# Kernel optimization log

Hardware: AMD Instinct MI355X
Metric: run time of the kernel (lower is better)

## Reference

```python
import jax, jax.numpy as jnp
import numpy as np

C = 1.0                      # curvature
PHI = 3.1415926 * 0.3        # Cosine phase (bias=False path)
ALPHA = 0.2                  # LeakyReLU negative slope
A_PARA = 0.5                 # a_para_GATLayer
EPS = 4e-3                   # float32 ball-projection epsilon (standard HGCN)
MIN_NORM = 1e-15
NEG_INF = -9e15              # matches -9000000000000000.0 in source


def project(x, c):
    # clamp points to lie inside the Poincare ball of curvature c
    norm = jnp.maximum(jnp.linalg.norm(x, axis=-1, keepdims=True), MIN_NORM)
    maxnorm = (1.0 - EPS) / jnp.sqrt(c)
    return jnp.where(norm > maxnorm, x / norm * maxnorm, x)


def artanh(x):
    return jnp.arctanh(jnp.clip(x, -1.0 + 1e-7, 1.0 - 1e-7))


def logmap0(p, c):
    # log map at the origin of the Poincare ball
    sqrt_c = c ** 0.5
    p_norm = jnp.maximum(jnp.linalg.norm(p, axis=-1, keepdims=True), MIN_NORM)
    return artanh(sqrt_c * p_norm) / (sqrt_c * p_norm) * p


def setup_inputs() -> dict:
    key = jax.random.key(0)
    k1, k2, k3, k4 = jax.random.split(key, 4)
    N, FIN, FOUT = 8192, 512, 128
    h = jax.random.normal(k1, (N, FIN), dtype=jnp.float32)
    adj = jax.random.randint(k2, (N, N), 0, 2, dtype=jnp.int32)
    # xavier_uniform with gain=1.414
    lim_w = 1.414 * np.sqrt(6.0 / (FIN + FOUT))
    W = jax.random.uniform(k3, (FIN, FOUT), jnp.float32, -lim_w, lim_w)
    lim_a = 1.414 * np.sqrt(6.0 / (2 * FOUT + 1))
    a = jax.random.uniform(k4, (2 * FOUT, 1), jnp.float32, -lim_a, lim_a)
    return {"h": h, "adj": adj, "W": W, "a": a}


def reference(h, adj, W, a):
    fout = W.shape[1]
    Wh = h @ W                                   # [N, F_out]
    Wh1 = Wh @ a[:fout]                          # [N, 1] source score
    Wh2 = Wh @ a[fout:]                          # [N, 1] target score
    e = jax.nn.leaky_relu(Wh1 + Wh2.T, ALPHA)    # [N, N]
    e = jnp.where(adj > 0, e, NEG_INF)
    attention = jax.nn.softmax(e, axis=1)        # dropout p=0 (eval): identity
    h_prime = attention @ Wh                     # [N, F_out]
    h_prime = logmap0(project(h_prime, C), C)
    # concat=True branch: ELU + a_para * A*cos(x + phi), A=1 (data_dim=-1)
    return jax.nn.elu(h_prime) + A_PARA * jnp.cos(h_prime + PHI)
```

## Files before the change

### kernel.cpp

```cpp
#include <hip/hip_runtime.h>
#include <hip/hip_bf16.h>
#include <math.h>

typedef short short8 __attribute__((ext_vector_type(8)));
typedef float f32x4 __attribute__((ext_vector_type(4)));

static constexpr int N = 8192;
static constexpr int FIN = 512;
static constexpr int FOUT = 128;
static constexpr float PHI = 3.1415926f * 0.3f;
static constexpr float A_PARA = 0.5f;
static constexpr float EPS_BALL = 4e-3f;
static constexpr float L2E = 1.4426950408889634f;

__device__ __forceinline__ unsigned short f2b(float f) {
    union { float f; unsigned u; } v; v.f = f;
    unsigned r = v.u + 0x7fffu + ((v.u >> 16) & 1u);
    return (unsigned short)(r >> 16);
}

__device__ __forceinline__ unsigned f2key(float x) {
    unsigned b = __float_as_uint(x);
    return (b & 0x80000000u) ? ~b : (b | 0x80000000u);
}
__device__ __forceinline__ float key2f(unsigned k) {
    unsigned b = (k & 0x80000000u) ? (k ^ 0x80000000u) : ~k;
    return __uint_as_float(b);
}

__device__ __forceinline__ short8 cvt8(float4 x0, float4 x1) {
    short8 r;
    r[0] = (short)f2b(x0.x); r[1] = (short)f2b(x0.y);
    r[2] = (short)f2b(x0.z); r[3] = (short)f2b(x0.w);
    r[4] = (short)f2b(x1.x); r[5] = (short)f2b(x1.y);
    r[6] = (short)f2b(x1.z); r[7] = (short)f2b(x1.w);
    return r;
}

__device__ __forceinline__ void cw(float* w, const int4 a, const float4 tv,
                                   float sA, float mA) {
    float z;
    z = sA + tv.x; w[0] = a.x > 0 ? __builtin_amdgcn_exp2f(fmaxf(z, 0.2f * z) - mA) : 0.f;
    z = sA + tv.y; w[1] = a.y > 0 ? __builtin_amdgcn_exp2f(fmaxf(z, 0.2f * z) - mA) : 0.f;
    z = sA + tv.z; w[2] = a.z > 0 ? __builtin_amdgcn_exp2f(fmaxf(z, 0.2f * z) - mA) : 0.f;
    z = sA + tv.w; w[3] = a.w > 0 ? __builtin_amdgcn_exp2f(fmaxf(z, 0.2f * z) - mA) : 0.f;
}

__global__ __launch_bounds__(256) void k0_wt(const float* __restrict__ W,
                                             unsigned short* __restrict__ Wt) {
    __shared__ float sh[32][33];
    const int t = threadIdx.x;
    const int k0 = (blockIdx.x >> 2) * 32, c0 = (blockIdx.x & 3) * 32;
    {
        int r = t >> 3, c4 = (t & 7) * 4;
        float4 v = *(const float4*)(W + (size_t)(k0 + r) * FOUT + c0 + c4);
        sh[r][c4] = v.x; sh[r][c4 + 1] = v.y; sh[r][c4 + 2] = v.z; sh[r][c4 + 3] = v.w;
    }
    __syncthreads();
    int cc = t >> 3, k4 = (t & 7) * 4;
    ushort4 o;
    o.x = f2b(sh[k4][cc]); o.y = f2b(sh[k4 + 1][cc]);
    o.z = f2b(sh[k4 + 2][cc]); o.w = f2b(sh[k4 + 3][cc]);
    *(ushort4*)(Wt + (size_t)(c0 + cc) * FIN + k0 + k4) = o;
}

__global__ __launch_bounds__(256) void k1_gemm(
    const float* __restrict__ h, const unsigned short* __restrict__ Wt,
    const float* __restrict__ a, unsigned short* __restrict__ whbt,
    float* __restrict__ s_out, float* __restrict__ t_out,
    unsigned* __restrict__ Tkey)
{
    __shared__ unsigned short hsb[2][32][72];
    __shared__ float sred[32][2], tred[32][2];
    const int t = threadIdx.x, lane = t & 63, wave = t >> 6;
    const int i0 = blockIdx.x * 32;
    const int wr = wave & 1, wc = wave >> 1;
    const int arow = lane & 15, g = lane >> 4;
    const int sr = t >> 3, sc = (t & 7) * 8;
    const float* hp = h + (size_t)(i0 + sr) * FIN + sc;

    float4 x0 = *(const float4*)hp, x1 = *(const float4*)(hp + 4);
    *(short8*)&hsb[0][sr][sc] = cvt8(x0, x1);
    __syncthreads();

    f32x4 acc[4];
    const f32x4 zz = {0.f, 0.f, 0.f, 0.f};
    #pragma unroll
    for (int cf = 0; cf < 4; ++cf) acc[cf] = zz;

    #pragma unroll 1
    for (int kt = 0; kt < 8; ++kt) {
        const int cur = kt & 1;
        float4 y0, y1;
        if (kt < 7) {
            y0 = *(const float4*)(hp + (kt + 1) * 64);
            y1 = *(const float4*)(hp + (kt + 1) * 64 + 4);
        }
        #pragma unroll
        for (int js = 0; js < 64; js += 32) {
            short8 af = *(const short8*)&hsb[cur][wr * 16 + arow][js + g * 8];
            #pragma unroll
            for (int cf = 0; cf < 4; ++cf) {
                const unsigned short* bp =
                    Wt + (size_t)(wc * 64 + cf * 16 + arow) * FIN + kt * 64 + js + g * 8;
                short8 bf = *(const short8*)bp;
                acc[cf] = __builtin_amdgcn_mfma_f32_16x16x32_bf16(af, bf, acc[cf], 0, 0, 0);
            }
        }
        if (kt < 7) {
            *(short8*)&hsb[cur ^ 1][sr][sc] = cvt8(y0, y1);
            __syncthreads();
        }
    }

    float a1v[4], a2v[4];
    #pragma unroll
    for (int cf = 0; cf < 4; ++cf) {
        int col = wc * 64 + cf * 16 + arow;
        a1v[cf] = a[col]; a2v[cf] = a[FOUT + col];
    }
    #pragma unroll
    for (int cf = 0; cf < 4; ++cf) {
        int col = wc * 64 + cf * 16 + arow;
        ushort4 o;
        o.x = f2b(acc[cf][0]); o.y = f2b(acc[cf][1]);
        o.z = f2b(acc[cf][2]); o.w = f2b(acc[cf][3]);
        *(ushort4*)(whbt + (size_t)col * N + i0 + wr * 16 + g * 4) = o;
    }
    #pragma unroll
    for (int q = 0; q < 4; ++q) {
        float sp = acc[0][q]*a1v[0] + acc[1][q]*a1v[1] + acc[2][q]*a1v[2] + acc[3][q]*a1v[3];
        float tp = acc[0][q]*a2v[0] + acc[1][q]*a2v[1] + acc[2][q]*a2v[2] + acc[3][q]*a2v[3];
        #pragma unroll
        for (int m = 1; m < 16; m <<= 1) {
            sp += __shfl_xor(sp, m, 16);
            tp += __shfl_xor(tp, m, 16);
        }
        if (arow == 0) {
            sred[wr * 16 + g * 4 + q][wc] = sp;
            tred[wr * 16 + g * 4 + q][wc] = tp;
        }
    }
    __syncthreads();
    if (t < 32) {
        float sp = (sred[t][0] + sred[t][1]) * L2E;
        float tp = (tred[t][0] + tred[t][1]) * L2E;
        s_out[i0 + t] = sp;
        t_out[i0 + t] = tp;
        float m = tp;
        #pragma unroll
        for (int d = 1; d < 32; d <<= 1) m = fmaxf(m, __shfl_xor(m, d, 32));
        if (t == 0) atomicMax(Tkey, f2key(m));
    }
}

__global__ __launch_bounds__(512, 4) void k3_attn(
    const int* __restrict__ adj, const unsigned short* __restrict__ whbt,
    const float* __restrict__ s_in, const float* __restrict__ t_in,
    const unsigned* __restrict__ Tkey,
    unsigned short* __restrict__ num_bf, float* __restrict__ num_f32,
    float* __restrict__ den_out, int slice_mode)
{
    __shared__ unsigned short bt[2][128][72];
    __shared__ float tl[1024];
    const int t = threadIdx.x, lane = t & 63, wave = t >> 6;
    const int jc = blockIdx.x & 7, it = blockIdx.x >> 3;
    const int i0 = it * 128, jbase = jc * 1024;

    tl[t] = t_in[jbase + t];
    tl[t + 512] = t_in[jbase + t + 512];

    const int arow = lane & 15, g = lane >> 4;
    const int grow = i0 + wave * 16 + arow;
    const float sA = s_in[grow];
    const float Tv = key2f(Tkey[0]);
    const float zT = sA + Tv;
    const float mA = fmaxf(zT, 0.2f * zT);
    const int* adjrow = adj + (size_t)grow * N;
    const int srow = t >> 2, scol = (t & 3) * 16;
    const unsigned short* sbase = whbt + (size_t)srow * N + jbase + scol;

    f32x4 acc[8];
    const f32x4 zz = {0.f, 0.f, 0.f, 0.f};
    #pragma unroll
    for (int c = 0; c < 8; ++c) acc[c] = zz;
    float den = 0.f;

    short8 sr0 = *(const short8*)sbase;
    short8 sr1 = *(const short8*)(sbase + 8);
    int4 av0 = *(const int4*)(adjrow + jbase + g * 8);
    int4 av1 = *(const int4*)(adjrow + jbase + g * 8 + 4);
    int4 av2 = *(const int4*)(adjrow + jbase + 32 + g * 8);
    int4 av3 = *(const int4*)(adjrow + jbase + 32 + g * 8 + 4);
    *(short8*)&bt[0][srow][scol]     = sr0;
    *(short8*)&bt[0][srow][scol + 8] = sr1;
    __syncthreads();

    #pragma unroll 1
    for (int jt = 0; jt < 16; ++jt) {
        const int cur = jt & 1, jl = jt * 64;
        float4 ta = *(const float4*)&tl[jl + g * 8];
        float4 tb = *(const float4*)&tl[jl + g * 8 + 4];
        float4 tc = *(const float4*)&tl[jl + 32 + g * 8];
        float4 td = *(const float4*)&tl[jl + 32 + g * 8 + 4];
        int4 an0, an1, an2, an3; short8 n0, n1;
        if (jt < 15) {
            const int* ap = adjrow + jbase + jl + 64;
            an0 = *(const int4*)(ap + g * 8);
            an1 = *(const int4*)(ap + g * 8 + 4);
            an2 = *(const int4*)(ap + 32 + g * 8);
            an3 = *(const int4*)(ap + 32 + g * 8 + 4);
            const unsigned short* p = sbase + (jt + 1) * 64;
            n0 = *(const short8*)p;
            n1 = *(const short8*)(p + 8);
        }
        float w[16];
        cw(&w[0],  av0, ta, sA, mA);
        cw(&w[4],  av1, tb, sA, mA);
        cw(&w[8],  av2, tc, sA, mA);
        cw(&w[12], av3, td, sA, mA);
        #pragma unroll
        for (int e = 0; e < 16; ++e) den += w[e];
        short8 af0, af1;
        #pragma unroll
        for (int e = 0; e < 8; ++e) {
            af0[e] = (short)f2b(w[e]);
            af1[e] = (short)f2b(w[8 + e]);
        }
        #pragma unroll
        for (int c = 0; c < 8; ++c) {
            short8 bf = *(const short8*)&bt[cur][c * 16 + arow][g * 8];
            acc[c] = __builtin_amdgcn_mfma_f32_16x16x32_bf16(af0, bf, acc[c], 0, 0, 0);
        }
        #pragma unroll
        for (int c = 0; c < 8; ++c) {
            short8 bf = *(const short8*)&bt[cur][c * 16 + arow][32 + g * 8];
            acc[c] = __builtin_amdgcn_mfma_f32_16x16x32_bf16(af1, bf, acc[c], 0, 0, 0);
        }
        if (jt < 15) {
            *(short8*)&bt[cur ^ 1][srow][scol]     = n0;
            *(short8*)&bt[cur ^ 1][srow][scol + 8] = n1;
            av0 = an0; av1 = an1; av2 = an2; av3 = an3;
            __syncthreads();
        }
    }

    den += __shfl_xor(den, 16, 64);
    den += __shfl_xor(den, 32, 64);
    if (g == 0) atomicAdd(&den_out[grow], den);

    const int orow0 = i0 + wave * 16;
    if (slice_mode) {
        unsigned short* dst = num_bf + (size_t)jc * ((size_t)N * FOUT);
        #pragma unroll
        for (int c = 0; c < 8; ++c)
            #pragma unroll
            for (int q = 0; q < 4; ++q)
                dst[(size_t)(orow0 + g * 4 + q) * FOUT + c * 16 + arow] = f2b(acc[c][q]);
    } else {
        #pragma unroll
        for (int c = 0; c < 8; ++c)
            #pragma unroll
            for (int q = 0; q < 4; ++q)
                atomicAdd(&num_f32[(size_t)(orow0 + g * 4 + q) * FOUT + c * 16 + arow], acc[c][q]);
    }
}

__global__ __launch_bounds__(256) void k4_epi(
    const unsigned short* __restrict__ numb, const float* __restrict__ numf,
    const float* __restrict__ den, float* __restrict__ out, int bfmode)
{
    const int row = blockIdx.x * 16 + (threadIdx.x >> 4);
    const int l = threadIdx.x & 15;
    const float inv = 1.0f / den[row];
    float v[8]; float ss = 0.f;
    #pragma unroll
    for (int c = 0; c < 8; ++c) {
        float x = 0.f;
        if (bfmode) {
            for (int s5 = 0; s5 < 8; ++s5) {
                unsigned b = numb[(size_t)s5 * N * FOUT + (size_t)row * FOUT + c * 16 + l];
                x += __uint_as_float(b << 16);
            }
        } else {
            x = numf[(size_t)row * FOUT + c * 16 + l];
        }
        v[c] = x * inv;
        ss += v[c] * v[c];
    }
    #pragma unroll
    for (int m = 1; m < 16; m <<= 1) ss += __shfl_xor(ss, m, 16);
    float nrm = sqrtf(ss);
    const float maxn = 1.0f - EPS_BALL;
    float scale1 = nrm > maxn ? maxn / nrm : 1.0f;
    float pn = fminf(nrm, maxn);
    float fac;
    if (pn < 1e-6f) fac = scale1;
    else fac = scale1 * (0.5f * __logf((1.f + pn) / (1.f - pn))) / pn;
    #pragma unroll
    for (int c = 0; c < 8; ++c) {
        float hv = v[c] * fac;
        float eluv = hv > 0.f ? hv : __expf(hv) - 1.f;
        out[(size_t)row * FOUT + c * 16 + l] = eluv + A_PARA * __cosf(hv + PHI);
    }
}

extern "C" void kernel_launch(void* const* d_in, const int* in_sizes, int n_in,
                              void* d_out, int out_size, void* d_ws, size_t ws_size,
                              hipStream_t stream) {
    const float* h   = (const float*)d_in[0];
    const int*   adj = (const int*)d_in[1];
    const float* W   = (const float*)d_in[2];
    const float* a   = (const float*)d_in[3];
    float* out = (float*)d_out;

    char* ws = (char*)d_ws;
    unsigned short* whbt = (unsigned short*)ws;
    size_t off = (size_t)N * FOUT * 2;
    unsigned short* Wt = (unsigned short*)(ws + off); off += (size_t)FOUT * FIN * 2;
    float* s  = (float*)(ws + off); off += (size_t)N * 4;
    float* tt = (float*)(ws + off); off += (size_t)N * 4;
    unsigned* Tkey = (unsigned*)(ws + off); off += 256;
    float* denb = (float*)(ws + off); off += (size_t)N * 4;
    const size_t slice_bytes = (size_t)N * FOUT * 2;
    const bool fast = ws_size >= off + 8 * slice_bytes;
    unsigned short* numb = fast ? (unsigned short*)(ws + off) : nullptr;

    hipMemsetAsync(Tkey, 0, 4, stream);
    hipMemsetAsync(denb, 0, (size_t)N * 4, stream);
    if (!fast) hipMemsetAsync(out, 0, (size_t)N * FOUT * 4, stream);

    k0_wt<<<64, 256, 0, stream>>>(W, Wt);
    k1_gemm<<<N / 32, 256, 0, stream>>>(h, Wt, a, whbt, s, tt, Tkey);
    k3_attn<<<512, 512, 0, stream>>>(adj, whbt, s, tt, Tkey, numb, out, denb, fast ? 1 : 0);
    k4_epi<<<N / 16, 256, 0, stream>>>(numb, out, denb, out, fast ? 1 : 0);
}
```

Baseline: 104.4 us.

## Fold memsets into W transpose, retile GEMM, deepen adj prefetch, vectorize epilogue

Zeroing of Tkey and the denominator buffer moves into the W-transpose kernel, which removes two memset launches. The projection GEMM now uses 16-row blocks with the whole K-slice of h staged in LDS and no inner barriers, giving twice as many blocks. The attention kernel prefetches adjacency two tiles ahead instead of one, at the cost of more registers. The epilogue reads bf16 slices and writes its output as 8-wide vectors instead of strided scalars.

```diff
diff --git a/kernel.cpp b/kernel.cpp
--- a/kernel.cpp
+++ b/kernel.cpp
@@ -47,7 +47,9 @@
 }
 
 __global__ __launch_bounds__(256) void k0_wt(const float* __restrict__ W,
-                                             unsigned short* __restrict__ Wt) {
+                                             unsigned short* __restrict__ Wt,
+                                             unsigned* __restrict__ Tkey,
+                                             float* __restrict__ denb) {
     __shared__ float sh[32][33];
     const int t = threadIdx.x;
     const int k0 = (blockIdx.x >> 2) * 32, c0 = (blockIdx.x & 3) * 32;
@@ -62,94 +64,84 @@
     o.x = f2b(sh[k4][cc]); o.y = f2b(sh[k4 + 1][cc]);
     o.z = f2b(sh[k4 + 2][cc]); o.w = f2b(sh[k4 + 3][cc]);
     *(ushort4*)(Wt + (size_t)(c0 + cc) * FIN + k0 + k4) = o;
-}
-
-__global__ __launch_bounds__(256) void k1_gemm(
+    if (blockIdx.x == 0) {
+        if (t == 0) Tkey[0] = 0u;
+        for (int i = t; i < N; i += 256) denb[i] = 0.f;
+    }
+}
+
+__global__ __launch_bounds__(256, 2) void k1_gemm(
     const float* __restrict__ h, const unsigned short* __restrict__ Wt,
     const float* __restrict__ a, unsigned short* __restrict__ whbt,
     float* __restrict__ s_out, float* __restrict__ t_out,
     unsigned* __restrict__ Tkey)
 {
-    __shared__ unsigned short hsb[2][32][72];
-    __shared__ float sred[32][2], tred[32][2];
-    const int t = threadIdx.x, lane = t & 63, wave = t >> 6;
-    const int i0 = blockIdx.x * 32;
-    const int wr = wave & 1, wc = wave >> 1;
+    __shared__ unsigned short hsb[16][520];
+    __shared__ float sred[16][4], tred[16][4];
+    const int t = threadIdx.x, lane = t & 63, wc = t >> 6;
+    const int i0 = blockIdx.x * 16;
     const int arow = lane & 15, g = lane >> 4;
-    const int sr = t >> 3, sc = (t & 7) * 8;
-    const float* hp = h + (size_t)(i0 + sr) * FIN + sc;
-
-    float4 x0 = *(const float4*)hp, x1 = *(const float4*)(hp + 4);
-    *(short8*)&hsb[0][sr][sc] = cvt8(x0, x1);
+
+    {
+        const int r = t >> 4, col0 = (t & 15) * 32;
+        const float* hp = h + (size_t)(i0 + r) * FIN + col0;
+        #pragma unroll
+        for (int u = 0; u < 4; ++u) {
+            float4 x0 = *(const float4*)(hp + u * 8);
+            float4 x1 = *(const float4*)(hp + u * 8 + 4);
+            *(short8*)&hsb[r][col0 + u * 8] = cvt8(x0, x1);
+        }
+    }
     __syncthreads();
 
-    f32x4 acc[4];
+    f32x4 acc[2];
     const f32x4 zz = {0.f, 0.f, 0.f, 0.f};
-    #pragma unroll
-    for (int cf = 0; cf < 4; ++cf) acc[cf] = zz;
-
-    #pragma unroll 1
-    for (int kt = 0; kt < 8; ++kt) {
-        const int cur = kt & 1;
-        float4 y0, y1;
-        if (kt < 7) {
-            y0 = *(const float4*)(hp + (kt + 1) * 64);
-            y1 = *(const float4*)(hp + (kt + 1) * 64 + 4);
-        }
-        #pragma unroll
-        for (int js = 0; js < 64; js += 32) {
-            short8 af = *(const short8*)&hsb[cur][wr * 16 + arow][js + g * 8];
-            #pragma unroll
-            for (int cf = 0; cf < 4; ++cf) {
-                const unsigned short* bp =
-                    Wt + (size_t)(wc * 64 + cf * 16 + arow) * FIN + kt * 64 + js + g * 8;
-                short8 bf = *(const short8*)bp;
-                acc[cf] = __builtin_amdgcn_mfma_f32_16x16x32_bf16(af, bf, acc[cf], 0, 0, 0);
-            }
-        }
-        if (kt < 7) {
-            *(short8*)&hsb[cur ^ 1][sr][sc] = cvt8(y0, y1);
-            __syncthreads();
-        }
-    }
-
-    float a1v[4], a2v[4];
-    #pragma unroll
-    for (int cf = 0; cf < 4; ++cf) {
-        int col = wc * 64 + cf * 16 + arow;
-        a1v[cf] = a[col]; a2v[cf] = a[FOUT + col];
-    }
-    #pragma unroll
-    for (int cf = 0; cf < 4; ++cf) {
-        int col = wc * 64 + cf * 16 + arow;
+    acc[0] = zz; acc[1] = zz;
+    const int col_0 = wc * 32 + arow;
+    const int col_1 = wc * 32 + 16 + arow;
+    const unsigned short* bp0 = Wt + (size_t)col_0 * FIN + g * 8;
+    const unsigned short* bp1 = Wt + (size_t)col_1 * FIN + g * 8;
+
+    #pragma unroll
+    for (int ks = 0; ks < 16; ++ks) {
+        short8 af = *(const short8*)&hsb[arow][ks * 32 + g * 8];
+        short8 b0 = *(const short8*)(bp0 + ks * 32);
+        short8 b1 = *(const short8*)(bp1 + ks * 32);
+        acc[0] = __builtin_amdgcn_mfma_f32_16x16x32_bf16(af, b0, acc[0], 0, 0, 0);
+        acc[1] = __builtin_amdgcn_mfma_f32_16x16x32_bf16(af, b1, acc[1], 0, 0, 0);
+    }
+
+    const float a10 = a[col_0], a11 = a[col_1];
+    const float a20 = a[FOUT + col_0], a21 = a[FOUT + col_1];
+    {
         ushort4 o;
-        o.x = f2b(acc[cf][0]); o.y = f2b(acc[cf][1]);
-        o.z = f2b(acc[cf][2]); o.w = f2b(acc[cf][3]);
-        *(ushort4*)(whbt + (size_t)col * N + i0 + wr * 16 + g * 4) = o;
+        o.x = f2b(acc[0][0]); o.y = f2b(acc[0][1]);
+        o.z = f2b(acc[0][2]); o.w = f2b(acc[0][3]);
+        *(ushort4*)(whbt + (size_t)col_0 * N + i0 + g * 4) = o;
+        o.x = f2b(acc[1][0]); o.y = f2b(acc[1][1]);
+        o.z = f2b(acc[1][2]); o.w = f2b(acc[1][3]);
+        *(ushort4*)(whbt + (size_t)col_1 * N + i0 + g * 4) = o;
     }
     #pragma unroll
     for (int q = 0; q < 4; ++q) {
-        float sp = acc[0][q]*a1v[0] + acc[1][q]*a1v[1] + acc[2][q]*a1v[2] + acc[3][q]*a1v[3];
-        float tp = acc[0][q]*a2v[0] + acc[1][q]*a2v[1] + acc[2][q]*a2v[2] + acc[3][q]*a2v[3];
+        float sp = acc[0][q] * a10 + acc[1][q] * a11;
+        float tp = acc[0][q] * a20 + acc[1][q] * a21;
         #pragma unroll
         for (int m = 1; m < 16; m <<= 1) {
             sp += __shfl_xor(sp, m, 16);
             tp += __shfl_xor(tp, m, 16);
         }
-        if (arow == 0) {
-            sred[wr * 16 + g * 4 + q][wc] = sp;
-            tred[wr * 16 + g * 4 + q][wc] = tp;
-        }
+        if (arow == 0) { sred[g * 4 + q][wc] = sp; tred[g * 4 + q][wc] = tp; }
     }
     __syncthreads();
-    if (t < 32) {
-        float sp = (sred[t][0] + sred[t][1]) * L2E;
-        float tp = (tred[t][0] + tred[t][1]) * L2E;
+    if (t < 16) {
+        float sp = (sred[t][0] + sred[t][1] + sred[t][2] + sred[t][3]) * L2E;
+        float tp = (tred[t][0] + tred[t][1] + tred[t][2] + tred[t][3]) * L2E;
         s_out[i0 + t] = sp;
         t_out[i0 + t] = tp;
         float m = tp;
         #pragma unroll
-        for (int d = 1; d < 32; d <<= 1) m = fmaxf(m, __shfl_xor(m, d, 32));
+        for (int d = 1; d < 16; d <<= 1) m = fmaxf(m, __shfl_xor(m, d, 16));
         if (t == 0) atomicMax(Tkey, f2key(m));
     }
 }
@@ -192,6 +184,10 @@
     int4 av1 = *(const int4*)(adjrow + jbase + g * 8 + 4);
     int4 av2 = *(const int4*)(adjrow + jbase + 32 + g * 8);
     int4 av3 = *(const int4*)(adjrow + jbase + 32 + g * 8 + 4);
+    int4 bv0 = *(const int4*)(adjrow + jbase + 64 + g * 8);
+    int4 bv1 = *(const int4*)(adjrow + jbase + 64 + g * 8 + 4);
+    int4 bv2 = *(const int4*)(adjrow + jbase + 96 + g * 8);
+    int4 bv3 = *(const int4*)(adjrow + jbase + 96 + g * 8 + 4);
     *(short8*)&bt[0][srow][scol]     = sr0;
     *(short8*)&bt[0][srow][scol + 8] = sr1;
     __syncthreads();
@@ -199,21 +195,24 @@
     #pragma unroll 1
     for (int jt = 0; jt < 16; ++jt) {
         const int cur = jt & 1, jl = jt * 64;
+        short8 n0, n1;
+        if (jt < 15) {
+            const unsigned short* p = sbase + (jt + 1) * 64;
+            n0 = *(const short8*)p;
+            n1 = *(const short8*)(p + 8);
+        }
+        int4 zv0, zv1, zv2, zv3;
+        if (jt < 14) {
+            const int* ap = adjrow + jbase + jl + 128;
+            zv0 = *(const int4*)(ap + g * 8);
+            zv1 = *(const int4*)(ap + g * 8 + 4);
+            zv2 = *(const int4*)(ap + 32 + g * 8);
+            zv3 = *(const int4*)(ap + 32 + g * 8 + 4);
+        }
         float4 ta = *(const float4*)&tl[jl + g * 8];
         float4 tb = *(const float4*)&tl[jl + g * 8 + 4];
         float4 tc = *(const float4*)&tl[jl + 32 + g * 8];
         float4 td = *(const float4*)&tl[jl + 32 + g * 8 + 4];
-        int4 an0, an1, an2, an3; short8 n0, n1;
-        if (jt < 15) {
-            const int* ap = adjrow + jbase + jl + 64;
-            an0 = *(const int4*)(ap + g * 8);
-            an1 = *(const int4*)(ap + g * 8 + 4);
-            an2 = *(const int4*)(ap + 32 + g * 8);
-            an3 = *(const int4*)(ap + 32 + g * 8 + 4);
-            const unsigned short* p = sbase + (jt + 1) * 64;
-            n0 = *(const short8*)p;
-            n1 = *(const short8*)(p + 8);
-        }
         float w[16];
         cw(&w[0],  av0, ta, sA, mA);
         cw(&w[4],  av1, tb, sA, mA);
@@ -240,7 +239,8 @@
         if (jt < 15) {
             *(short8*)&bt[cur ^ 1][srow][scol]     = n0;
             *(short8*)&bt[cur ^ 1][srow][scol + 8] = n1;
-            av0 = an0; av1 = an1; av2 = an2; av3 = an3;
+            av0 = bv0; av1 = bv1; av2 = bv2; av3 = bv3;
+            if (jt < 14) { bv0 = zv0; bv1 = zv1; bv2 = zv2; bv3 = zv3; }
             __syncthreads();
         }
     }
@@ -271,23 +271,24 @@
     const float* __restrict__ den, float* __restrict__ out, int bfmode)
 {
     const int row = blockIdx.x * 16 + (threadIdx.x >> 4);
-    const int l = threadIdx.x & 15;
+    const int col0 = (threadIdx.x & 15) * 8;
     const float inv = 1.0f / den[row];
-    float v[8]; float ss = 0.f;
-    #pragma unroll
-    for (int c = 0; c < 8; ++c) {
-        float x = 0.f;
-        if (bfmode) {
-            for (int s5 = 0; s5 < 8; ++s5) {
-                unsigned b = numb[(size_t)s5 * N * FOUT + (size_t)row * FOUT + c * 16 + l];
-                x += __uint_as_float(b << 16);
-            }
-        } else {
-            x = numf[(size_t)row * FOUT + c * 16 + l];
-        }
-        v[c] = x * inv;
-        ss += v[c] * v[c];
-    }
+    float v[8] = {};
+    if (bfmode) {
+        #pragma unroll 1
+        for (int s5 = 0; s5 < 8; ++s5) {
+            short8 b = *(const short8*)(numb + (size_t)s5 * N * FOUT + (size_t)row * FOUT + col0);
+            #pragma unroll
+            for (int c = 0; c < 8; ++c)
+                v[c] += __uint_as_float(((unsigned)(unsigned short)b[c]) << 16);
+        }
+    } else {
+        #pragma unroll
+        for (int c = 0; c < 8; ++c) v[c] = numf[(size_t)row * FOUT + col0 + c];
+    }
+    float ss = 0.f;
+    #pragma unroll
+    for (int c = 0; c < 8; ++c) { v[c] *= inv; ss += v[c] * v[c]; }
     #pragma unroll
     for (int m = 1; m < 16; m <<= 1) ss += __shfl_xor(ss, m, 16);
     float nrm = sqrtf(ss);
@@ -297,12 +298,16 @@
     float fac;
     if (pn < 1e-6f) fac = scale1;
     else fac = scale1 * (0.5f * __logf((1.f + pn) / (1.f - pn))) / pn;
+    float o[8];
     #pragma unroll
     for (int c = 0; c < 8; ++c) {
         float hv = v[c] * fac;
         float eluv = hv > 0.f ? hv : __expf(hv) - 1.f;
-        out[(size_t)row * FOUT + c * 16 + l] = eluv + A_PARA * __cosf(hv + PHI);
-    }
+        o[c] = eluv + A_PARA * __cosf(hv + PHI);
+    }
+    float* op = out + (size_t)row * FOUT + col0;
+    *(float4*)op = make_float4(o[0], o[1], o[2], o[3]);
+    *(float4*)(op + 4) = make_float4(o[4], o[5], o[6], o[7]);
 }
 
 extern "C" void kernel_launch(void* const* d_in, const int* in_sizes, int n_in,
@@ -326,12 +331,10 @@
     const bool fast = ws_size >= off + 8 * slice_bytes;
     unsigned short* numb = fast ? (unsigned short*)(ws + off) : nullptr;
 
-    hipMemsetAsync(Tkey, 0, 4, stream);
-    hipMemsetAsync(denb, 0, (size_t)N * 4, stream);
     if (!fast) hipMemsetAsync(out, 0, (size_t)N * FOUT * 4, stream);
 
-    k0_wt<<<64, 256, 0, stream>>>(W, Wt);
-    k1_gemm<<<N / 32, 256, 0, stream>>>(h, Wt, a, whbt, s, tt, Tkey);
+    k0_wt<<<64, 256, 0, stream>>>(W, Wt, Tkey, denb);
+    k1_gemm<<<N / 16, 256, 0, stream>>>(h, Wt, a, whbt, s, tt, Tkey);
     k3_attn<<<512, 512, 0, stream>>>(adj, whbt, s, tt, Tkey, numb, out, denb, fast ? 1 : 0);
     k4_epi<<<N / 16, 256, 0, stream>>>(numb, out, denb, out, fast ? 1 : 0);
 }
```

Result: slower. 112.9 us (+8.2%).
